# Kernel optimization log

Hardware: AMD Instinct MI355X
Metric: run time of the kernel (lower is better)

## Reference

```python
import jax, jax.numpy as jnp
import numpy as np

N_RES = 4096
N_PAIRS = 500000

def setup_inputs() -> dict:
    key = jax.random.key(0)
    k1, k2, k3 = jax.random.split(key, 3)
    ca_coords = jax.random.normal(k1, (N_RES, 3), dtype=jnp.float32) * 10.0
    K = jax.random.uniform(k2, (N_RES, N_RES), dtype=jnp.float32)
    pairs = jax.random.randint(k3, (N_PAIRS, 2), 0, N_RES, dtype=jnp.int64)
    return {"ca_coords": ca_coords, "K": K, "pairs": pairs}


def _reconstruct_backbone(ca):
    # vectorized version of reconstruct_backbone_atoms
    n = ca.shape[0]
    vec = ca[1:] - ca[:-1]                                  # (n-1,3)
    unit = vec / (jnp.linalg.norm(vec, axis=-1, keepdims=True) + 1e-8)
    # N atoms: n_coords[i] = ca[i] - 0.38*unit(ca[i]-ca[i-1]); n_coords[0] uses unit[0]
    n_coords = jnp.concatenate([ca[:1] - 0.38 * unit[:1], ca[1:] - 0.38 * unit], axis=0)
    # C atoms: c_coords[i] = ca[i] + 0.38*unit(ca[i+1]-ca[i]); c_coords[-1] uses unit[-1]
    c_coords = jnp.concatenate([ca[:-1] + 0.38 * unit, ca[-1:] + 0.38 * unit[-1:]], axis=0)
    # O atoms: perpendicular to (C-CA, N-CA) plane, last residue special-cased
    vec_n = n_coords[:-1] - ca[:-1]
    vec_c = c_coords[:-1] - ca[:-1]
    perp = jnp.cross(vec_c, vec_n)
    pnorm = jnp.linalg.norm(perp, axis=-1, keepdims=True)
    perp = jnp.where(pnorm > 1e-6, perp / jnp.maximum(pnorm, 1e-12), perp)
    o_body = c_coords[:-1] + 1.24 * perp
    o_last = c_coords[-1:] + jnp.array([[0.0, 1.24, 0.0]], dtype=ca.dtype)
    o_coords = jnp.concatenate([o_body, o_last], axis=0)
    return n_coords, c_coords, o_coords


def _pairwise_dist(x, y):
    # safe cdist: sqrt clamped so diagonal zeros stay differentiable
    sq = jnp.sum((x[:, None, :] - y[None, :, :]) ** 2, axis=-1)
    return jnp.sqrt(jnp.maximum(sq, 1e-12))


def reference(ca_coords, K, pairs):
    n = ca_coords.shape[0]

    # --- bond energy (weight=30): mean((|ca[i+1]-ca[i]| - 3.8)^2) ---
    d_bond = jnp.linalg.norm(ca_coords[1:] - ca_coords[:-1], axis=-1)
    e_bond = 30.0 * jnp.mean((d_bond - 3.8) ** 2)

    # --- clash energy (weight=50): mean(relu(3.2 - d_pair)^2) ---
    dv = ca_coords[pairs[:, 0]] - ca_coords[pairs[:, 1]]
    d_pair = jnp.sqrt(jnp.maximum(jnp.sum(dv ** 2, axis=-1), 1e-12))
    e_clash = 50.0 * jnp.mean(jax.nn.relu(3.2 - d_pair) ** 2)

    # --- contact energy (weight=5): mean((D - 8*(1-K))^2) over full NxN ---
    D = _pairwise_dist(ca_coords, ca_coords)
    target = 8.0 * (1.0 - K)
    e_contact = 5.0 * jnp.mean((D - target) ** 2)

    # --- hydrogen bond energy (weight=4) from reconstructed backbone ---
    n_coords, c_coords, o_coords = _reconstruct_backbone(ca_coords)
    ideal = 2.95
    hb = jnp.float32(0.0)
    # double loop i, j in [i+2, i+6) -> offsets 2..5, vectorized per offset
    for off in (2, 3, 4, 5):
        d = jnp.linalg.norm(o_coords[: n - off] - n_coords[off:], axis=-1)
        pen = jnp.exp(-(((d - ideal) / 0.3) ** 2))
        hb = hb - 0.5 * jnp.sum(jnp.where((d > 2.5) & (d < 3.5), pen, 0.0))
    e_hb = 4.0 * hb / (n * n)

    return e_bond + e_clash + e_contact + e_hb
```

## Files before the change

kernel.cpp:

```cpp
#include <hip/hip_runtime.h>
#include <math.h>

#define NRES   4096
#define GRID   768
#define TROWS  4
#define NTILES (NRES / TROWS)
#define HB_BLOCKS (NRES / 256)
#define PSTRIDE (GRID * 256)

typedef int i32x2 __attribute__((ext_vector_type(2)));

__device__ __forceinline__ float wave_sum(float v) {
#pragma unroll
    for (int off = 32; off > 0; off >>= 1) v += __shfl_down(v, off, 64);
    return v;
}

__device__ __forceinline__ float fsqrt(float x) { return __builtin_amdgcn_sqrtf(x); }

__device__ __forceinline__ float c4(float4 kv, float4 cx, float4 cy, float4 cz,
                                    float xi, float yi, float zi, float s) {
    float dx, dy, dz, D, t;
    dx = xi - cx.x; dy = yi - cy.x; dz = zi - cz.x;
    D  = fsqrt(fmaf(dx, dx, fmaf(dy, dy, dz * dz)));
    t  = fmaf(8.f, kv.x, D - 8.f);
    s  = fmaf(t, t, s);

    dx = xi - cx.y; dy = yi - cy.y; dz = zi - cz.y;
    D  = fsqrt(fmaf(dx, dx, fmaf(dy, dy, dz * dz)));
    t  = fmaf(8.f, kv.y, D - 8.f);
    s  = fmaf(t, t, s);

    dx = xi - cx.z; dy = yi - cy.z; dz = zi - cz.z;
    D  = fsqrt(fmaf(dx, dx, fmaf(dy, dy, dz * dz)));
    t  = fmaf(8.f, kv.z, D - 8.f);
    s  = fmaf(t, t, s);

    dx = xi - cx.w; dy = yi - cy.w; dz = zi - cz.w;
    D  = fsqrt(fmaf(dx, dx, fmaf(dy, dy, dz * dz)));
    t  = fmaf(8.f, kv.w, D - 8.f);
    s  = fmaf(t, t, s);
    return s;
}

__global__ __launch_bounds__(256, 3) void energy_kernel(const float* __restrict__ ca,
                                                        const float* __restrict__ K,
                                                        const int* __restrict__ pairs,
                                                        float4* __restrict__ partial,
                                                        int npairs) {
    __shared__ float sx[NRES], sy[NRES], sz[NRES];
    __shared__ float red[4][4];
    const int tid = threadIdx.x;
    const int b   = blockIdx.x;

    const int pbase = b * 256 + tid;
    const i32x2* pairs2 = (const i32x2*)pairs;
    i32x2 pr0 = pairs2[pbase];
    i32x2 pr1 = pairs2[pbase + PSTRIDE];
    const bool has2 = (pbase + 2 * PSTRIDE) < npairs;
    i32x2 pr2 = has2 ? pairs2[pbase + 2 * PSTRIDE] : (i32x2){0, 0};

    for (int j = tid; j < NRES; j += 256) {
        sx[j] = ca[3 * j + 0];
        sy[j] = ca[3 * j + 1];
        sz[j] = ca[3 * j + 2];
    }
    __syncthreads();

    float contact = 0.f;
    for (int t = b; t < NTILES; t += GRID) {
        const int rbase = t * TROWS;
        float xi[TROWS], yi[TROWS], zi[TROWS];
#pragma unroll
        for (int r = 0; r < TROWS; ++r) {
            xi[r] = sx[rbase + r]; yi[r] = sy[rbase + r]; zi[r] = sz[rbase + r];
        }

        const float* Kt = K + (size_t)rbase * NRES;
        const int j0 = tid << 2;
        float4 va[TROWS], vb[TROWS];
#pragma unroll
        for (int r = 0; r < TROWS; ++r)
            va[r] = *(const float4*)(Kt + (size_t)r * NRES + j0);

#pragma unroll
        for (int c = 0; c < 4; ++c) {
            const int jc = j0 + (c << 10);
            float4* cur = (c & 1) ? vb : va;
            float4* nxt = (c & 1) ? va : vb;
            if (c < 3) {
                const int jn = j0 + ((c + 1) << 10);
#pragma unroll
                for (int r = 0; r < TROWS; ++r)
                    nxt[r] = *(const float4*)(Kt + (size_t)r * NRES + jn);
            }
            const float4 cx = *(const float4*)&sx[jc];
            const float4 cy = *(const float4*)&sy[jc];
            const float4 cz = *(const float4*)&sz[jc];
#pragma unroll
            for (int r = 0; r < TROWS; ++r)
                contact = c4(cur[r], cx, cy, cz, xi[r], yi[r], zi[r], contact);
        }
    }

    float clash = 0.f;
    {
        float dx, dy, dz, d, r;
        dx = sx[pr0.x] - sx[pr0.y]; dy = sy[pr0.x] - sy[pr0.y]; dz = sz[pr0.x] - sz[pr0.y];
        d = fsqrt(fmaxf(fmaf(dx, dx, fmaf(dy, dy, dz * dz)), 1e-12f));
        r = fmaxf(3.2f - d, 0.f); clash = fmaf(r, r, clash);

        dx = sx[pr1.x] - sx[pr1.y]; dy = sy[pr1.x] - sy[pr1.y]; dz = sz[pr1.x] - sz[pr1.y];
        d = fsqrt(fmaxf(fmaf(dx, dx, fmaf(dy, dy, dz * dz)), 1e-12f));
        r = fmaxf(3.2f - d, 0.f); clash = fmaf(r, r, clash);

        if (has2) {
            dx = sx[pr2.x] - sx[pr2.y]; dy = sy[pr2.x] - sy[pr2.y]; dz = sz[pr2.x] - sz[pr2.y];
            d = fsqrt(fmaxf(fmaf(dx, dx, fmaf(dy, dy, dz * dz)), 1e-12f));
            r = fmaxf(3.2f - d, 0.f); clash = fmaf(r, r, clash);
        }
    }

    float bond = 0.f, hb = 0.f;
    if (b < HB_BLOCKS) {
        const int i = b * 256 + tid;
        const int n = NRES;

        if (i < n - 1) {
            float dx = sx[i+1]-sx[i], dy = sy[i+1]-sy[i], dz = sz[i+1]-sz[i];
            float d  = sqrtf(fmaf(dx, dx, fmaf(dy, dy, dz * dz)));
            float t  = d - 3.8f;
            bond = t * t;
        }

        if (i < n - 2) {
            float cax = sx[i], cay = sy[i], caz = sz[i];
            float vx = sx[i+1]-cax, vy = sy[i+1]-cay, vz = sz[i+1]-caz;
            float inv = 1.f / (sqrtf(vx*vx + vy*vy + vz*vz) + 1e-8f);
            float ux = vx*inv, uy = vy*inv, uz = vz*inv;

            float upx, upy, upz;
            if (i == 0) { upx = ux; upy = uy; upz = uz; }
            else {
                float wx = cax-sx[i-1], wy = cay-sy[i-1], wz = caz-sz[i-1];
                float inv2 = 1.f / (sqrtf(wx*wx + wy*wy + wz*wz) + 1e-8f);
                upx = wx*inv2; upy = wy*inv2; upz = wz*inv2;
            }

            float vcx = 0.38f*ux,  vcy = 0.38f*uy,  vcz = 0.38f*uz;
            float vnx = -0.38f*upx, vny = -0.38f*upy, vnz = -0.38f*upz;
            float px = vcy*vnz - vcz*vny;
            float py = vcz*vnx - vcx*vnz;
            float pz = vcx*vny - vcy*vnx;
            float pn = sqrtf(px*px + py*py + pz*pz);
            if (pn > 1e-6f) {
                float ipn = 1.f / fmaxf(pn, 1e-12f);
                px *= ipn; py *= ipn; pz *= ipn;
            }
            float ox = cax + vcx + 1.24f*px;
            float oy = cay + vcy + 1.24f*py;
            float oz = caz + vcz + 1.24f*pz;

#pragma unroll
            for (int off = 2; off <= 5; ++off) {
                int jj = i + off;
                if (jj < n) {
                    float cjx = sx[jj], cjy = sy[jj], cjz = sz[jj];
                    float qx = cjx-sx[jj-1], qy = cjy-sy[jj-1], qz = cjz-sz[jj-1];
                    float invq = 1.f / (sqrtf(qx*qx + qy*qy + qz*qz) + 1e-8f);
                    float njx = cjx - 0.38f*qx*invq;
                    float njy = cjy - 0.38f*qy*invq;
                    float njz = cjz - 0.38f*qz*invq;
                    float ddx = ox-njx, ddy = oy-njy, ddz = oz-njz;
                    float d = sqrtf(ddx*ddx + ddy*ddy + ddz*ddz);
                    if (d > 2.5f && d < 3.5f) {
                        float z = (d - 2.95f) * (1.0f / 0.3f);
                        hb -= 0.5f * expf(-z*z);
                    }
                }
            }
        }
    }

    float vbo = wave_sum(bond);
    float vcl = wave_sum(clash);
    float vco = wave_sum(contact);
    float vhb = wave_sum(hb);
    const int wave = tid >> 6;
    if ((tid & 63) == 0) {
        red[wave][0] = vbo; red[wave][1] = vcl; red[wave][2] = vco; red[wave][3] = vhb;
    }
    __syncthreads();
    if (tid == 0) {
        float4 o;
        o.x = red[0][0] + red[1][0] + red[2][0] + red[3][0];
        o.y = red[0][1] + red[1][1] + red[2][1] + red[3][1];
        o.z = red[0][2] + red[1][2] + red[2][2] + red[3][2];
        o.w = red[0][3] + red[1][3] + red[2][3] + red[3][3];
        partial[b] = o;
    }
}

__global__ __launch_bounds__(256) void finalize_kernel(const float4* __restrict__ partial,
                                                       float* __restrict__ out,
                                                       int n, int npairs) {
    __shared__ float red[4][4];
    const int tid = threadIdx.x;
    float vb = 0.f, vc = 0.f, vk = 0.f, vh = 0.f;
#pragma unroll
    for (int s = 0; s < GRID; s += 256) {
        float4 a = partial[tid + s];
        vb += a.x; vc += a.y; vk += a.z; vh += a.w;
    }
    vb = wave_sum(vb); vc = wave_sum(vc); vk = wave_sum(vk); vh = wave_sum(vh);
    const int wave = tid >> 6;
    if ((tid & 63) == 0) {
        red[wave][0] = vb; red[wave][1] = vc; red[wave][2] = vk; red[wave][3] = vh;
    }
    __syncthreads();
    if (tid == 0) {
        float bond    = red[0][0] + red[1][0] + red[2][0] + red[3][0];
        float clash   = red[0][1] + red[1][1] + red[2][1] + red[3][1];
        float contact = red[0][2] + red[1][2] + red[2][2] + red[3][2];
        float hb      = red[0][3] + red[1][3] + red[2][3] + red[3][3];
        float inv_nn  = 1.f / ((float)n * (float)n);
        out[0] = 30.f * bond / (float)(n - 1)
               + 50.f * clash / (float)npairs
               + 5.f  * contact * inv_nn
               + 4.f  * hb * inv_nn;
    }
}

extern "C" void kernel_launch(void* const* d_in, const int* in_sizes, int n_in,
                              void* d_out, int out_size, void* d_ws, size_t ws_size,
                              hipStream_t stream) {
    const float* ca    = (const float*)d_in[0];
    const float* K     = (const float*)d_in[1];
    const int*   pairs = (const int*)d_in[2];
    float* out = (float*)d_out;
    float4* partial = (float4*)d_ws;

    int n      = in_sizes[0] / 3;
    int npairs = in_sizes[2] / 2;

    energy_kernel<<<GRID, 256, 0, stream>>>(ca, K, pairs, partial, npairs);
    finalize_kernel<<<1, 256, 0, stream>>>(partial, out, n, npairs);
}
```

Measured before the change: 100.4 us.

## Use 512-thread blocks with contiguous 5-6 row contact slabs per block

Doubles the block size to 512 threads and gives each block one contiguous slab of 6 or 5 rows of K (256 blocks take 6 rows, 512 take 5), so every one of the 4096 rows is covered once. Each thread now holds fixed column coordinates for two float4 column groups in registers and prefetches the next row's K values, instead of looping over 4-row tiles with column chunks. The clash work drops to two pairs per thread and the per-block reduction now handles 8 waves. The goal is to cut per-tile overhead and LDS traffic for column coordinates, though the uneven 6-vs-5 row split leaves some load imbalance and the larger blocks change occupancy.

```diff
diff --git a/kernel.cpp b/kernel.cpp
--- a/kernel.cpp
+++ b/kernel.cpp
@@ -1,12 +1,11 @@
 #include <hip/hip_runtime.h>
 #include <math.h>
 
-#define NRES   4096
-#define GRID   768
-#define TROWS  4
-#define NTILES (NRES / TROWS)
-#define HB_BLOCKS (NRES / 256)
-#define PSTRIDE (GRID * 256)
+#define NRES 4096
+#define GRID 768
+#define BLOCK 512
+#define HB_BLOCKS 8
+#define NTHREADS (GRID * BLOCK)
 
 typedef int i32x2 __attribute__((ext_vector_type(2)));
 
@@ -43,65 +42,67 @@
     return s;
 }
 
-__global__ __launch_bounds__(256, 3) void energy_kernel(const float* __restrict__ ca,
-                                                        const float* __restrict__ K,
-                                                        const int* __restrict__ pairs,
-                                                        float4* __restrict__ partial,
-                                                        int npairs) {
+template <int R>
+__device__ __forceinline__ float contact_rows(const float* __restrict__ K, int row0,
+                                              const float* sx, const float* sy,
+                                              const float* sz, int tid) {
+    const int j0 = tid << 2;
+    const int j1 = (tid + BLOCK) << 2;
+    const float* Kt = K + (size_t)row0 * NRES;
+
+    const float4 cxa = *(const float4*)&sx[j0];
+    const float4 cya = *(const float4*)&sy[j0];
+    const float4 cza = *(const float4*)&sz[j0];
+    const float4 cxb = *(const float4*)&sx[j1];
+    const float4 cyb = *(const float4*)&sy[j1];
+    const float4 czb = *(const float4*)&sz[j1];
+
+    float s = 0.f;
+    float4 ka = *(const float4*)(Kt + j0);
+    float4 kb = *(const float4*)(Kt + j1);
+#pragma unroll
+    for (int r = 0; r < R; ++r) {
+        float4 na = ka, nb = kb;
+        if (r + 1 < R) {
+            na = *(const float4*)(Kt + (size_t)(r + 1) * NRES + j0);
+            nb = *(const float4*)(Kt + (size_t)(r + 1) * NRES + j1);
+        }
+        const float xi = sx[row0 + r];
+        const float yi = sy[row0 + r];
+        const float zi = sz[row0 + r];
+        s = c4(ka, cxa, cya, cza, xi, yi, zi, s);
+        s = c4(kb, cxb, cyb, czb, xi, yi, zi, s);
+        ka = na; kb = nb;
+    }
+    return s;
+}
+
+__global__ __launch_bounds__(BLOCK, 6) void energy_kernel(const float* __restrict__ ca,
+                                                          const float* __restrict__ K,
+                                                          const int* __restrict__ pairs,
+                                                          float4* __restrict__ partial,
+                                                          int npairs) {
     __shared__ float sx[NRES], sy[NRES], sz[NRES];
-    __shared__ float red[4][4];
+    __shared__ float red[8][4];
     const int tid = threadIdx.x;
     const int b   = blockIdx.x;
 
-    const int pbase = b * 256 + tid;
+    const int g = b * BLOCK + tid;
     const i32x2* pairs2 = (const i32x2*)pairs;
-    i32x2 pr0 = pairs2[pbase];
-    i32x2 pr1 = pairs2[pbase + PSTRIDE];
-    const bool has2 = (pbase + 2 * PSTRIDE) < npairs;
-    i32x2 pr2 = has2 ? pairs2[pbase + 2 * PSTRIDE] : (i32x2){0, 0};
-
-    for (int j = tid; j < NRES; j += 256) {
+    i32x2 pr0 = pairs2[g];
+    const bool has1 = (g + NTHREADS) < npairs;
+    i32x2 pr1 = has1 ? pairs2[g + NTHREADS] : (i32x2){0, 0};
+
+    for (int j = tid; j < NRES; j += BLOCK) {
         sx[j] = ca[3 * j + 0];
         sy[j] = ca[3 * j + 1];
         sz[j] = ca[3 * j + 2];
     }
     __syncthreads();
 
-    float contact = 0.f;
-    for (int t = b; t < NTILES; t += GRID) {
-        const int rbase = t * TROWS;
-        float xi[TROWS], yi[TROWS], zi[TROWS];
-#pragma unroll
-        for (int r = 0; r < TROWS; ++r) {
-            xi[r] = sx[rbase + r]; yi[r] = sy[rbase + r]; zi[r] = sz[rbase + r];
-        }
-
-        const float* Kt = K + (size_t)rbase * NRES;
-        const int j0 = tid << 2;
-        float4 va[TROWS], vb[TROWS];
-#pragma unroll
-        for (int r = 0; r < TROWS; ++r)
-            va[r] = *(const float4*)(Kt + (size_t)r * NRES + j0);
-
-#pragma unroll
-        for (int c = 0; c < 4; ++c) {
-            const int jc = j0 + (c << 10);
-            float4* cur = (c & 1) ? vb : va;
-            float4* nxt = (c & 1) ? va : vb;
-            if (c < 3) {
-                const int jn = j0 + ((c + 1) << 10);
-#pragma unroll
-                for (int r = 0; r < TROWS; ++r)
-                    nxt[r] = *(const float4*)(Kt + (size_t)r * NRES + jn);
-            }
-            const float4 cx = *(const float4*)&sx[jc];
-            const float4 cy = *(const float4*)&sy[jc];
-            const float4 cz = *(const float4*)&sz[jc];
-#pragma unroll
-            for (int r = 0; r < TROWS; ++r)
-                contact = c4(cur[r], cx, cy, cz, xi[r], yi[r], zi[r], contact);
-        }
-    }
+    float contact;
+    if (b < 256) contact = contact_rows<6>(K, b * 6, sx, sy, sz, tid);
+    else         contact = contact_rows<5>(K, 1536 + (b - 256) * 5, sx, sy, sz, tid);
 
     float clash = 0.f;
     {
@@ -110,12 +111,8 @@
         d = fsqrt(fmaxf(fmaf(dx, dx, fmaf(dy, dy, dz * dz)), 1e-12f));
         r = fmaxf(3.2f - d, 0.f); clash = fmaf(r, r, clash);
 
-        dx = sx[pr1.x] - sx[pr1.y]; dy = sy[pr1.x] - sy[pr1.y]; dz = sz[pr1.x] - sz[pr1.y];
-        d = fsqrt(fmaxf(fmaf(dx, dx, fmaf(dy, dy, dz * dz)), 1e-12f));
-        r = fmaxf(3.2f - d, 0.f); clash = fmaf(r, r, clash);
-
-        if (has2) {
-            dx = sx[pr2.x] - sx[pr2.y]; dy = sy[pr2.x] - sy[pr2.y]; dz = sz[pr2.x] - sz[pr2.y];
+        if (has1) {
+            dx = sx[pr1.x] - sx[pr1.y]; dy = sy[pr1.x] - sy[pr1.y]; dz = sz[pr1.x] - sz[pr1.y];
             d = fsqrt(fmaxf(fmaf(dx, dx, fmaf(dy, dy, dz * dz)), 1e-12f));
             r = fmaxf(3.2f - d, 0.f); clash = fmaf(r, r, clash);
         }
@@ -123,7 +120,7 @@
 
     float bond = 0.f, hb = 0.f;
     if (b < HB_BLOCKS) {
-        const int i = b * 256 + tid;
+        const int i = b * BLOCK + tid;
         const int n = NRES;
 
         if (i < n - 1) {
@@ -192,11 +189,11 @@
     }
     __syncthreads();
     if (tid == 0) {
-        float4 o;
-        o.x = red[0][0] + red[1][0] + red[2][0] + red[3][0];
-        o.y = red[0][1] + red[1][1] + red[2][1] + red[3][1];
-        o.z = red[0][2] + red[1][2] + red[2][2] + red[3][2];
-        o.w = red[0][3] + red[1][3] + red[2][3] + red[3][3];
+        float4 o = {0.f, 0.f, 0.f, 0.f};
+#pragma unroll
+        for (int w = 0; w < 8; ++w) {
+            o.x += red[w][0]; o.y += red[w][1]; o.z += red[w][2]; o.w += red[w][3];
+        }
         partial[b] = o;
     }
 }
@@ -243,6 +240,6 @@
     int n      = in_sizes[0] / 3;
     int npairs = in_sizes[2] / 2;
 
-    energy_kernel<<<GRID, 256, 0, stream>>>(ca, K, pairs, partial, npairs);
+    energy_kernel<<<GRID, BLOCK, 0, stream>>>(ca, K, pairs, partial, npairs);
     finalize_kernel<<<1, 256, 0, stream>>>(partial, out, n, npairs);
 }
```

New measurement: 105.0 us. +4.6%, slower.
